# Kernel tuning notes

Hardware: AMD Instinct MI355X
Metric: run time of the kernel (lower is better)

## Reference

```python
import jax, jax.numpy as jnp
import numpy as np

H = W = 256
FX = FY = 1.0
CX = CY = 0.5


def setup_inputs() -> dict:
    key = jax.random.key(0)
    k1, k2, k3 = jax.random.split(key, 3)
    B, N = 8, 500000
    points = jax.random.normal(k1, (B, N, 3), dtype=jnp.float32)
    densities = jax.random.uniform(k2, (B, N, 1), dtype=jnp.float32)
    depth = jax.random.uniform(k3, (B, 1, H, W), dtype=jnp.float32)
    return {"points": points, "densities": densities, "depth": depth}


def project_points_to_depth(points, densities):
    # points: [B,N,3], densities: [B,N,1] -> depth grid [B,1,H,W]
    B, N, _ = points.shape
    x = points[:, :, 0]
    y = points[:, :, 1]
    z = points[:, :, 2]
    # pinhole projection; .long() in torch truncates toward zero, as does astype(int32)
    u = jnp.clip(((FX * x / z + CX) * W).astype(jnp.int32), 0, W - 1)  # [B,N]
    v = jnp.clip(((FY * y / z + CY) * H).astype(jnp.int32), 0, H - 1)  # [B,N]
    d = densities[:, :, 0]
    val = jnp.where(d > 0.5, z * d, jnp.float32(0.0))  # conditional contribution
    idx = v * W + u  # flat pixel index [B,N]
    flat = jnp.zeros((B, H * W), dtype=points.dtype)
    flat = flat.at[jnp.arange(B)[:, None], idx].add(val)  # batched scatter-add
    return flat.reshape(B, 1, H, W)


def reference(points, densities, depth):
    projected = project_points_to_depth(points, densities)
    mask = projected > 0
    diff2 = jnp.where(mask, (projected - depth) ** 2, jnp.float32(0.0))
    count = jnp.maximum(jnp.sum(mask), 1)
    # F.mse_loss over masked elements == mean of squared diffs where mask
    return jnp.sum(diff2) / count.astype(diff2.dtype)
```

## Files before the change

### kernel.cpp

```cpp
#include <hip/hip_runtime.h>

#define HH 256
#define WW 256
#define HWSZ (HH * WW)

#define GRIDX 32
#define TPB 1024
#define NSLOTS 1022

typedef float vf4 __attribute__((ext_vector_type(4)));

__global__ __launch_bounds__(TPB, 4) void scatter_k(
    const float* __restrict__ pts, const float* __restrict__ dens,
    float* __restrict__ flat, float* __restrict__ accum,
    int* __restrict__ done, int N)
{
    __shared__ float lds[NSLOTS];
    for (int s = threadIdx.x; s < NSLOTS; s += TPB) lds[s] = 0.0f;

    if (blockIdx.x == 0 && blockIdx.y == 0 && threadIdx.x == 0) {
        accum[0] = 0.0f;
        ((int*)accum)[1] = 0;
        *done = 0;
    }
    __syncthreads();

    int b = blockIdx.y;
    const float* pb = pts + (size_t)b * N * 3;
    const float* db = dens + (size_t)b * N;
    float* out = flat + (size_t)b * HWSZ;

    int ngroups = N >> 2;
    int gpb = (ngroups + GRIDX - 1) / GRIDX;
    int gbase = blockIdx.x * gpb;
    int gend = min(gbase + gpb, ngroups);
    int last = ngroups - 1;
    const vf4* p4 = (const vf4*)pb;
    const vf4* d4 = (const vf4*)db;

    int g0 = gbase + threadIdx.x;
    int g1 = g0 + TPB, g2 = g0 + 2 * TPB, g3 = g0 + 3 * TPB;
    int c0 = min(g0, last), c1 = min(g1, last),
        c2 = min(g2, last), c3 = min(g3, last);

    const vf4* pa0 = p4 + 3 * c0; const vf4* pa1 = p4 + 3 * c1;
    const vf4* pa2 = p4 + 3 * c2; const vf4* pa3 = p4 + 3 * c3;
    const vf4* da0 = d4 + c0;     const vf4* da1 = d4 + c1;
    const vf4* da2 = d4 + c2;     const vf4* da3 = d4 + c3;

    vf4 A0, B0, C0, D0, A1, B1, C1, D1;
    vf4 A2, B2, C2, D2, A3, B3, C3, D3;
#define GLOAD(dst, base, off) \
    asm volatile("global_load_dwordx4 %0, %1, off offset:" #off \
                 : "=&v"(dst) : "v"(base) : "memory")
    GLOAD(A0, pa0, 0); GLOAD(B0, pa0, 16); GLOAD(C0, pa0, 32);
    GLOAD(A1, pa1, 0); GLOAD(B1, pa1, 16); GLOAD(C1, pa1, 32);
    GLOAD(A2, pa2, 0); GLOAD(B2, pa2, 16); GLOAD(C2, pa2, 32);
    GLOAD(A3, pa3, 0); GLOAD(B3, pa3, 16); GLOAD(C3, pa3, 32);
    GLOAD(D0, da0, 0); GLOAD(D1, da1, 0);
    GLOAD(D2, da2, 0); GLOAD(D3, da3, 0);
#undef GLOAD
    asm volatile("s_waitcnt vmcnt(0)"
                 : "+v"(A0), "+v"(B0), "+v"(C0), "+v"(D0),
                   "+v"(A1), "+v"(B1), "+v"(C1), "+v"(D1),
                   "+v"(A2), "+v"(B2), "+v"(C2), "+v"(D2),
                   "+v"(A3), "+v"(B3), "+v"(C3), "+v"(D3));
    __builtin_amdgcn_sched_barrier(0);

    if (g0 >= gend) { D0 = (vf4)0.0f; }
    if (g1 >= gend) { D1 = (vf4)0.0f; }
    if (g2 >= gend) { D2 = (vf4)0.0f; }
    if (g3 >= gend) { D3 = (vf4)0.0f; }

    float corner[4] = {0.0f, 0.0f, 0.0f, 0.0f};

    auto proc = [&](const vf4& a, const vf4& bb, const vf4& c,
                    const vf4& dd) {
        float xs[4] = {a.x, a.w, bb.z, c.y};
        float ys[4] = {a.y, bb.x, bb.w, c.z};
        float zs[4] = {a.z, bb.y, c.x, c.w};
        float ds[4] = {dd.x, dd.y, dd.z, dd.w};

        #pragma unroll
        for (int k = 0; k < 4; k++) {
            float d = ds[k];
            float z = zs[k];
            bool acc = d > 0.5f;
            float r = __builtin_amdgcn_rcpf(z) * 256.0f;
            float uf = fmaf(xs[k], r, 128.0f);
            float vf = fmaf(ys[k], r, 128.0f);
            int u = (int)fminf(fmaxf(uf, 0.0f), 255.0f);
            int v = (int)fminf(fmaxf(vf, 0.0f), 255.0f);
            float val = z * d;

            bool u0 = (u == 0), u255 = (u == 255);
            bool v0 = (v == 0), v255 = (v == 255);
            bool ub = u0 | u255;
            bool vb = v0 | v255;
            bool iscorner = acc & ub & vb;
            bool isborder = acc & (ub ^ vb);
            bool isinter  = acc & !ub & !vb;

            int ci = (v255 ? 2 : 0) | (u255 ? 1 : 0);
            corner[0] += (iscorner && ci == 0) ? val : 0.0f;
            corner[1] += (iscorner && ci == 1) ? val : 0.0f;
            corner[2] += (iscorner && ci == 2) ? val : 0.0f;
            corner[3] += (iscorner && ci == 3) ? val : 0.0f;

            int slot = v0 ? u : (v255 ? 256 + u : (u0 ? 511 + v : 767 + v));
            if (isborder) atomicAdd(&lds[slot], val);
            if (isinter)  atomicAdd(out + v * WW + u, val);
        }
    };

    proc(A0, B0, C0, D0);
    proc(A1, B1, C1, D1);
    proc(A2, B2, C2, D2);
    proc(A3, B3, C3, D3);

    #pragma unroll
    for (int j = 0; j < 4; j++) {
        float v = corner[j];
        #pragma unroll
        for (int off = 32; off > 0; off >>= 1) v += __shfl_down(v, off);
        if ((threadIdx.x & 63) == 0) {
            const int cslot[4] = {0, 255, 256, 511};
            atomicAdd(&lds[cslot[j]], v);
        }
    }

    __syncthreads();
    for (int s = threadIdx.x; s < NSLOTS; s += TPB) {
        float v = lds[s];
        if (v != 0.0f) {
            int u, vv;
            if (s < 256)      { vv = 0;        u = s; }
            else if (s < 512) { vv = 255;      u = s - 256; }
            else if (s < 768) { u = 0;         vv = s - 512 + 1; }
            else              { u = 255;       vv = s - 768 + 1; }
            atomicAdd(out + vv * WW + u, v);
        }
    }
}

#define LBLOCKS 128
#define ELEMS_PER_THREAD 4
__global__ __launch_bounds__(256) void loss_k(
    const float* __restrict__ flat, const float* __restrict__ depth,
    float* __restrict__ accum, int* __restrict__ done,
    float* __restrict__ out, int total4, int nblocks)
{
    const float4* f4 = (const float4*)flat;
    const float4* z4 = (const float4*)depth;

    int i0 = blockIdx.x * blockDim.x + threadIdx.x;
    int stride = gridDim.x * blockDim.x;

    float4 p[ELEMS_PER_THREAD], q[ELEMS_PER_THREAD];
    bool ok[ELEMS_PER_THREAD];
    #pragma unroll
    for (int k = 0; k < ELEMS_PER_THREAD; k++) {
        int i = i0 + k * stride;
        ok[k] = i < total4;
        if (ok[k]) { p[k] = f4[i]; q[k] = z4[i]; }
    }
    float s = 0.0f;
    int c = 0;
    for (int i = i0 + ELEMS_PER_THREAD * stride; i < total4; i += stride) {
        float4 pp = f4[i];
        float4 qq = z4[i];
        if (pp.x > 0.0f) { float df = pp.x - qq.x; s += df * df; c++; }
        if (pp.y > 0.0f) { float df = pp.y - qq.y; s += df * df; c++; }
        if (pp.z > 0.0f) { float df = pp.z - qq.z; s += df * df; c++; }
        if (pp.w > 0.0f) { float df = pp.w - qq.w; s += df * df; c++; }
    }
    #pragma unroll
    for (int k = 0; k < ELEMS_PER_THREAD; k++) {
        if (ok[k]) {
            float4 pp = p[k], qq = q[k];
            if (pp.x > 0.0f) { float df = pp.x - qq.x; s += df * df; c++; }
            if (pp.y > 0.0f) { float df = pp.y - qq.y; s += df * df; c++; }
            if (pp.z > 0.0f) { float df = pp.z - qq.z; s += df * df; c++; }
            if (pp.w > 0.0f) { float df = pp.w - qq.w; s += df * df; c++; }
        }
    }

    #pragma unroll
    for (int off = 32; off > 0; off >>= 1) {
        s += __shfl_down(s, off);
        c += __shfl_down(c, off);
    }

    __shared__ float bsum[4];
    __shared__ int bcnt[4];
    int wave = threadIdx.x >> 6;
    if ((threadIdx.x & 63) == 0) { bsum[wave] = s; bcnt[wave] = c; }
    __syncthreads();
    if (threadIdx.x == 0) {
        float ts = bsum[0] + bsum[1] + bsum[2] + bsum[3];
        int tc = bcnt[0] + bcnt[1] + bcnt[2] + bcnt[3];
        atomicAdd(accum, ts);
        atomicAdd((int*)accum + 1, tc);
        __threadfence();
        int old = atomicAdd(done, 1);
        if (old == nblocks - 1) {
            float fs = atomicAdd(accum, 0.0f);
            int fc = atomicAdd((int*)accum + 1, 0);
            out[0] = fs / (float)(fc >= 1 ? fc : 1);
        }
    }
}

extern "C" void kernel_launch(void* const* d_in, const int* in_sizes, int n_in,
                              void* d_out, int out_size, void* d_ws, size_t ws_size,
                              hipStream_t stream) {
    const float* pts   = (const float*)d_in[0];
    const float* dens  = (const float*)d_in[1];
    const float* depth = (const float*)d_in[2];
    float* out = (float*)d_out;

    int B = in_sizes[2] / HWSZ;
    int N = in_sizes[0] / (3 * B);

    float* flat  = (float*)d_ws;
    float* accum = flat + (size_t)B * HWSZ;
    int*   done  = (int*)(accum + 16);

    dim3 sgrid(GRIDX, B);
    scatter_k<<<sgrid, TPB, 0, stream>>>(pts, dens, flat, accum, done, N);

    int total4 = B * HWSZ / 4;
    loss_k<<<dim3(LBLOCKS), 256, 0, stream>>>(flat, depth, accum, done, out,
                                              total4, LBLOCKS);
}
```

Before: 115.0 us.

## Stage per-block border sums and reduce them inside the loss kernel

The scatter kernel no longer flushes its LDS border and corner accumulators to the global depth grid with atomics. Each block now writes its 1022 slot values to a private staging buffer with plain stores. The loss kernel then sums the 32 partials per slot and adds the border pixels' squared errors directly. This removes the contended global atomics on the 1020 border pixels, at the cost of extra staging traffic and a hardcoded batch size of 8 in the loss kernel.

```diff
diff --git a/kernel.cpp b/kernel.cpp
--- a/kernel.cpp
+++ b/kernel.cpp
@@ -7,13 +7,14 @@
 #define GRIDX 32
 #define TPB 1024
 #define NSLOTS 1022
+#define SSTRIDE 1024
 
 typedef float vf4 __attribute__((ext_vector_type(4)));
 
 __global__ __launch_bounds__(TPB, 4) void scatter_k(
     const float* __restrict__ pts, const float* __restrict__ dens,
-    float* __restrict__ flat, float* __restrict__ accum,
-    int* __restrict__ done, int N)
+    float* __restrict__ flat, float* __restrict__ stage,
+    float* __restrict__ accum, int* __restrict__ done, int N)
 {
     __shared__ float lds[NSLOTS];
     for (int s = threadIdx.x; s < NSLOTS; s += TPB) lds[s] = 0.0f;
@@ -130,25 +131,17 @@
     }
 
     __syncthreads();
-    for (int s = threadIdx.x; s < NSLOTS; s += TPB) {
-        float v = lds[s];
-        if (v != 0.0f) {
-            int u, vv;
-            if (s < 256)      { vv = 0;        u = s; }
-            else if (s < 512) { vv = 255;      u = s - 256; }
-            else if (s < 768) { u = 0;         vv = s - 512 + 1; }
-            else              { u = 255;       vv = s - 768 + 1; }
-            atomicAdd(out + vv * WW + u, v);
-        }
-    }
+    float* mystage = stage + ((size_t)b * GRIDX + blockIdx.x) * SSTRIDE;
+    for (int s = threadIdx.x; s < NSLOTS; s += TPB) mystage[s] = lds[s];
 }
 
 #define LBLOCKS 128
 #define ELEMS_PER_THREAD 4
 __global__ __launch_bounds__(256) void loss_k(
     const float* __restrict__ flat, const float* __restrict__ depth,
-    float* __restrict__ accum, int* __restrict__ done,
-    float* __restrict__ out, int total4, int nblocks)
+    const float* __restrict__ stage, float* __restrict__ accum,
+    int* __restrict__ done, float* __restrict__ out,
+    int total4, int nblocks)
 {
     const float4* f4 = (const float4*)flat;
     const float4* z4 = (const float4*)depth;
@@ -182,6 +175,26 @@
             if (pp.y > 0.0f) { float df = pp.y - qq.y; s += df * df; c++; }
             if (pp.z > 0.0f) { float df = pp.z - qq.z; s += df * df; c++; }
             if (pp.w > 0.0f) { float df = pp.w - qq.w; s += df * df; c++; }
+        }
+    }
+
+    if (i0 < 8 * NSLOTS) {
+        int b = i0 / NSLOTS;
+        int sl = i0 - b * NSLOTS;
+        const float* bs = stage + (size_t)b * GRIDX * SSTRIDE + sl;
+        float tot = 0.0f;
+        #pragma unroll 8
+        for (int k = 0; k < GRIDX; k++) tot += bs[(size_t)k * SSTRIDE];
+        int u, vv;
+        if (sl < 256)      { vv = 0;        u = sl; }
+        else if (sl < 512) { vv = 255;      u = sl - 256; }
+        else if (sl < 768) { u = 0;         vv = sl - 512 + 1; }
+        else               { u = 255;       vv = sl - 768 + 1; }
+        if (tot > 0.0f) {
+            float dq = depth[(size_t)b * HWSZ + vv * WW + u];
+            float df = tot - dq;
+            s += df * df;
+            c++;
         }
     }
 
@@ -225,11 +238,13 @@
     float* flat  = (float*)d_ws;
     float* accum = flat + (size_t)B * HWSZ;
     int*   done  = (int*)(accum + 16);
+    float* stage = accum + 64;
 
     dim3 sgrid(GRIDX, B);
-    scatter_k<<<sgrid, TPB, 0, stream>>>(pts, dens, flat, accum, done, N);
+    scatter_k<<<sgrid, TPB, 0, stream>>>(pts, dens, flat, stage, accum,
+                                         done, N);
 
     int total4 = B * HWSZ / 4;
-    loss_k<<<dim3(LBLOCKS), 256, 0, stream>>>(flat, depth, accum, done, out,
-                                              total4, LBLOCKS);
+    loss_k<<<dim3(LBLOCKS), 256, 0, stream>>>(flat, depth, stage, accum,
+                                              done, out, total4, LBLOCKS);
 }
```

Measured after the change: 114.1 us. No clear change (-0.8%).
